# Kernel tuning notes

Hardware: AMD Instinct MI355X
Metric: run time of the kernel (lower is better)

The kernel has to match this reference:

```python
import jax, jax.numpy as jnp
import numpy as np

D_MODEL = 256
SCALE = jnp.sqrt(jnp.float32(D_MODEL))


def setup_inputs() -> dict:
    key = jax.random.key(0)
    kq, kk, kv = jax.random.split(key, 3)
    B, S, D = 4, 4096, D_MODEL
    Q = jax.random.normal(kq, (B, S, D), dtype=jnp.float32)
    K = jax.random.normal(kk, (B, S, D), dtype=jnp.float32)
    V = jax.random.normal(kv, (B, S, D), dtype=jnp.float32)
    return {"Q": Q, "K": K, "V": V}


def reference(Q, K, V):
    # scores: (B, S, S) = Q @ K^T / sqrt(d_model)
    scores = jnp.einsum('bqd,bkd->bqk', Q, K) / SCALE
    attn = jax.nn.softmax(scores, axis=-1)
    # output: (B, S, D)
    return jnp.einsum('bqk,bkd->bqd', attn, V)
```

## Files before the change

### kernel.cpp

```cpp
#include <hip/hip_runtime.h>
#include <hip/hip_bf16.h>
#include <stdint.h>

#define S_LEN 4096
#define D_DIM 256
#define NBATCH 4
#define NKT 64
#define NSUP 32

typedef unsigned short u16;
typedef float  f32x4  __attribute__((ext_vector_type(4)));
typedef __bf16 bf16x8 __attribute__((ext_vector_type(8)));
typedef __bf16 bf16x4 __attribute__((ext_vector_type(4)));
typedef short  s16x8  __attribute__((ext_vector_type(8)));
typedef short  s16x4  __attribute__((ext_vector_type(4)));

__device__ __forceinline__ f32x4 mfma16(bf16x8 a, bf16x8 b, f32x4 c) {
  return __builtin_amdgcn_mfma_f32_16x16x32_bf16(a, b, c, 0, 0, 0);
}

__device__ __forceinline__ s16x4 cvt4(float x, float y, float z, float w) {
  bf16x4 b;
  b[0] = (__bf16)x; b[1] = (__bf16)y; b[2] = (__bf16)z; b[3] = (__bf16)w;
  return __builtin_bit_cast(s16x4, b);
}

__global__ void convert_bf16_kernel(const float* __restrict__ in,
                                    u16* __restrict__ out, int n4) {
  int i = blockIdx.x * blockDim.x + threadIdx.x;
  if (i >= n4) return;
  float4 f = reinterpret_cast<const float4*>(in)[i];
  reinterpret_cast<s16x4*>(out)[i] = cvt4(f.x, f.y, f.z, f.w);
}


__device__ __forceinline__
void compute_tile(const char* KsB, const char* vpA, const char* vpB,
                  const bf16x8 (&qf)[8], f32x4 (&acc)[16],
                  float& m_run, float& l_run, int g, int h)
{
  const f32x4 fz = {0.f, 0.f, 0.f, 0.f};

  f32x4 st[4];
  __builtin_amdgcn_s_setprio(1);
  #pragma unroll
  for (int t = 0; t < 4; ++t) {
    f32x4 a = fz;
    const int row = t * 16 + h;
    const int sw  = (row & 7) << 4;
    #pragma unroll
    for (int dc = 0; dc < 8; ++dc) {
      s16x8 kfrag = *reinterpret_cast<const s16x8*>(KsB + row * 512 + ((dc * 64 + g * 16) ^ sw));
      a = mfma16(__builtin_bit_cast(bf16x8, kfrag), qf[dc], a);
    }
    st[t] = a;
  }
  __builtin_amdgcn_s_setprio(0);

  float sv[16];
  #pragma unroll
  for (int t = 0; t < 4; ++t) {
    sv[t * 4 + 0] = st[t][0]; sv[t * 4 + 1] = st[t][1];
    sv[t * 4 + 2] = st[t][2]; sv[t * 4 + 3] = st[t][3];
  }
  float tmax = sv[0];
  #pragma unroll
  for (int i = 1; i < 16; ++i) tmax = fmaxf(tmax, sv[i]);
  tmax = fmaxf(tmax, __shfl_xor(tmax, 16));
  tmax = fmaxf(tmax, __shfl_xor(tmax, 32));

  if (!__all(tmax <= m_run + 8.0f)) {
    const float mnew  = fmaxf(m_run, tmax);
    const float alpha = __expf(m_run - mnew);
    l_run *= alpha;
    const float af0 = __shfl(alpha, g * 4 + 0);
    const float af1 = __shfl(alpha, g * 4 + 1);
    const float af2 = __shfl(alpha, g * 4 + 2);
    const float af3 = __shfl(alpha, g * 4 + 3);
    #pragma unroll
    for (int dt = 0; dt < 16; ++dt) {
      acc[dt][0] *= af0; acc[dt][1] *= af1; acc[dt][2] *= af2; acc[dt][3] *= af3;
    }
    m_run = mnew;
  }

  float psum = 0.f;
  #pragma unroll
  for (int i = 0; i < 16; ++i) { sv[i] = __expf(sv[i] - m_run); psum += sv[i]; }
  psum += __shfl_xor(psum, 16);
  psum += __shfl_xor(psum, 32);
  l_run += psum;

  bf16x8 pa0, pa1;
  #pragma unroll
  for (int j = 0; j < 8; ++j) { pa0[j] = (__bf16)sv[j]; pa1[j] = (__bf16)sv[8 + j]; }

  __builtin_amdgcn_s_setprio(1);
  #pragma unroll
  for (int dt = 0; dt < 16; ++dt) {
    s16x8 v0 = *reinterpret_cast<const s16x8*>(vpA + dt * 2048);
    s16x8 v1 = *reinterpret_cast<const s16x8*>(vpB + dt * 2048);
    acc[dt] = mfma16(pa0, __builtin_bit_cast(bf16x8, v0), acc[dt]);
    acc[dt] = mfma16(pa1, __builtin_bit_cast(bf16x8, v1), acc[dt]);
  }
  __builtin_amdgcn_s_setprio(0);
}

__device__ __forceinline__
void stage_tile(int T, const u16* ksrc, char* kdst,
                const u16* vsrc, char* VtB, int Xw, int dcq)
{
  const size_t nb = (size_t)T * 64 * D_DIM;
  s16x8 kreg[8], vlo[4], vhi[4];
  #pragma unroll
  for (int i = 0; i < 8; ++i)
    kreg[i] = *reinterpret_cast<const s16x8*>(ksrc + nb + (size_t)i * 8 * D_DIM);
  #pragma unroll
  for (int r = 0; r < 4; ++r) {
    const u16* s = vsrc + nb + (size_t)r * D_DIM;
    vlo[r] = *reinterpret_cast<const s16x8*>(s);
    vhi[r] = *reinterpret_cast<const s16x8*>(s + 8);
  }
  #pragma unroll
  for (int i = 0; i < 8; ++i)
    *reinterpret_cast<s16x8*>(kdst + i * 4096) = kreg[i];
  #pragma unroll
  for (int j = 0; j < 8; ++j) {
    s16x4 c0, c1;
    c0[0] = vlo[0][j]; c0[1] = vlo[1][j]; c0[2] = vlo[2][j]; c0[3] = vlo[3][j];
    c1[0] = vhi[0][j]; c1[1] = vhi[1][j]; c1[2] = vhi[2][j]; c1[3] = vhi[3][j];
    const int d0 = dcq * 16 + j;
    const int d1 = d0 + 8;
    *reinterpret_cast<s16x4*>(VtB + d0 * 128 + (Xw ^ ((d0 & 7) << 4))) = c0;
    *reinterpret_cast<s16x4*>(VtB + d1 * 128 + (Xw ^ ((d1 & 7) << 4))) = c1;
  }
}

template<bool USE_WS>
__global__ __launch_bounds__(512, 1)
void attn_fwd_kernel(const float* __restrict__ Qg, const void* __restrict__ Kp,
                     const void* __restrict__ Vp, float* __restrict__ Og)
{
  __shared__ __align__(16) char smem[131072];

  const int wg   = blockIdx.x;
  const int swz  = (wg & 7) * 32 + (wg >> 3);
  const int b    = swz >> 6;
  const int qt   = swz & 63;
  const int tid  = threadIdx.x;
  const int wave = tid >> 6;
  const int lane = tid & 63;
  const int g    = lane >> 4;
  const int h    = lane & 15;
  const int gid  = tid >> 8;
  const int ltid = tid & 255;
  const int wq   = wave & 3;

  const int kb  = ltid & 15;
  const int dcq = ltid >> 4;
  const int Xw  = 32 * (kb & 3) + 8 * (kb >> 2);

  char* KsB = smem + gid * 65536;
  char* VtB = KsB + 32768;

  const int qbase = qt * 64 + wq * 16;

  bf16x8 qf[8];
  {
    const float* qrow = Qg + ((size_t)b * S_LEN + qbase + h) * D_DIM;
    #pragma unroll
    for (int dc = 0; dc < 8; ++dc) {
      float4 f0 = *reinterpret_cast<const float4*>(qrow + dc * 32 + g * 8);
      float4 f1 = *reinterpret_cast<const float4*>(qrow + dc * 32 + g * 8 + 4);
      bf16x8 q;
      q[0] = (__bf16)(f0.x * 0.0625f); q[1] = (__bf16)(f0.y * 0.0625f);
      q[2] = (__bf16)(f0.z * 0.0625f); q[3] = (__bf16)(f0.w * 0.0625f);
      q[4] = (__bf16)(f1.x * 0.0625f); q[5] = (__bf16)(f1.y * 0.0625f);
      q[6] = (__bf16)(f1.z * 0.0625f); q[7] = (__bf16)(f1.w * 0.0625f);
      qf[dc] = q;
    }
  }

  f32x4 acc[16];
  const f32x4 fz = {0.f, 0.f, 0.f, 0.f};
  #pragma unroll
  for (int i = 0; i < 16; ++i) acc[i] = fz;
  float m_run = -1e30f;
  float l_run = 0.f;

  const char* vpA = VtB + h * 128 + ((32 * g)      ^ ((h & 7) << 4));
  const char* vpB = VtB + h * 128 + ((32 * g + 16) ^ ((h & 7) << 4));

  if constexpr (USE_WS) {
    const u16* Kb = (const u16*)Kp + (size_t)b * S_LEN * D_DIM;
    const u16* Vb = (const u16*)Vp + (size_t)b * S_LEN * D_DIM;

    const u16* ksrc = Kb + (size_t)(ltid >> 5) * D_DIM + (ltid & 31) * 8;
    char*      kdst = KsB + (ltid >> 5) * 512 + (((ltid & 31) * 16) ^ ((ltid >> 5) << 4));
    const u16* vsrc = Vb + (size_t)(kb * 4) * D_DIM + dcq * 16;

    if (gid == 0) stage_tile(0, ksrc, kdst, vsrc, VtB, Xw, dcq);
    __syncthreads();

    for (int s = 0; s < NSUP; ++s) {
      if (gid == 0) compute_tile(KsB, vpA, vpB, qf, acc, m_run, l_run, g, h);
      else          stage_tile(2 * s + 1, ksrc, kdst, vsrc, VtB, Xw, dcq);
      __syncthreads();
      if (gid == 0) { if (s < NSUP - 1) stage_tile(2 * s + 2, ksrc, kdst, vsrc, VtB, Xw, dcq); }
      else          compute_tile(KsB, vpA, vpB, qf, acc, m_run, l_run, g, h);
      __syncthreads();
    }

  } else {
    const float* Kf = (const float*)Kp + (size_t)b * S_LEN * D_DIM;
    const float* Vf = (const float*)Vp + (size_t)b * S_LEN * D_DIM;
    for (int s = 0; s < NSUP; ++s) {
      const int kt = 2 * s + gid;
      __syncthreads();
      #pragma unroll
      for (int i = 0; i < 16; ++i) {
        int flat = i * 256 + ltid;
        int kk = flat >> 6;
        int d  = (flat & 63) * 4;
        float4 fk = *reinterpret_cast<const float4*>(Kf + (size_t)(kt * 64 + kk) * D_DIM + d);
        *reinterpret_cast<s16x4*>(KsB + kk * 512 + ((d * 2) ^ ((kk & 7) << 4))) = cvt4(fk.x, fk.y, fk.z, fk.w);
      }
      {
        s16x8 lo[4], hi[4];
        #pragma unroll
        for (int r = 0; r < 4; ++r) {
          const float* src = Vf + (size_t)(kt * 64 + kb * 4 + r) * D_DIM + dcq * 16;
          float4 f0 = *reinterpret_cast<const float4*>(src);
          float4 f1 = *reinterpret_cast<const float4*>(src + 4);
          float4 f2 = *reinterpret_cast<const float4*>(src + 8);
          float4 f3 = *reinterpret_cast<const float4*>(src + 12);
          lo[r] = __builtin_shufflevector(cvt4(f0.x, f0.y, f0.z, f0.w),
                                          cvt4(f1.x, f1.y, f1.z, f1.w), 0, 1, 2, 3, 4, 5, 6, 7);
          hi[r] = __builtin_shufflevector(cvt4(f2.x, f2.y, f2.z, f2.w),
                                          cvt4(f3.x, f3.y, f3.z, f3.w), 0, 1, 2, 3, 4, 5, 6, 7);
        }
        #pragma unroll
        for (int j = 0; j < 8; ++j) {
          s16x4 c0, c1;
          c0[0] = lo[0][j]; c0[1] = lo[1][j]; c0[2] = lo[2][j]; c0[3] = lo[3][j];
          c1[0] = hi[0][j]; c1[1] = hi[1][j]; c1[2] = hi[2][j]; c1[3] = hi[3][j];
          const int d0 = dcq * 16 + j;
          const int d1 = d0 + 8;
          *reinterpret_cast<s16x4*>(VtB + d0 * 128 + (Xw ^ ((d0 & 7) << 4))) = c0;
          *reinterpret_cast<s16x4*>(VtB + d1 * 128 + (Xw ^ ((d1 & 7) << 4))) = c1;
        }
      }
      __syncthreads();
      compute_tile(KsB, vpA, vpB, qf, acc, m_run, l_run, g, h);
    }
  }

  __syncthreads();
  float2* mlM = reinterpret_cast<float2*>(smem + 65536);
  if (gid == 1) {
    const int bw = wave - 4;
    char* base = smem + bw * 16384 + lane * 256;
    #pragma unroll
    for (int dt = 0; dt < 16; ++dt) {
      float4 v; v.x = acc[dt][0]; v.y = acc[dt][1]; v.z = acc[dt][2]; v.w = acc[dt][3];
      *reinterpret_cast<float4*>(base + (dt * 16 ^ ((lane & 7) << 4))) = v;
    }
    if (g == 0) { float2 ml; ml.x = m_run; ml.y = l_run; mlM[bw * 16 + h] = ml; }
  }
  __syncthreads();
  if (gid == 0) {
    const float2 ml = mlM[wave * 16 + h];
    const float mB = ml.x, lB = ml.y;
    const float m  = fmaxf(m_run, mB);
    const float sA = __expf(m_run - m);
    const float sB = __expf(mB - m);
    const float l  = l_run * sA + lB * sB;
    float aA[4], aB[4], inv[4];
    #pragma unroll
    for (int r = 0; r < 4; ++r) {
      aA[r]  = __shfl(sA, g * 4 + r);
      aB[r]  = __shfl(sB, g * 4 + r);
      inv[r] = 1.f / __shfl(l, g * 4 + r);
    }
    const char* base = smem + wave * 16384 + lane * 256;
    float* orow0 = Og + ((size_t)b * S_LEN + qbase) * D_DIM;
    #pragma unroll
    for (int dt = 0; dt < 16; ++dt) {
      float4 ab = *reinterpret_cast<const float4*>(base + (dt * 16 ^ ((lane & 7) << 4)));
      orow0[(size_t)(g * 4 + 0) * D_DIM + h + dt * 16] = (acc[dt][0] * aA[0] + ab.x * aB[0]) * inv[0];
      orow0[(size_t)(g * 4 + 1) * D_DIM + h + dt * 16] = (acc[dt][1] * aA[1] + ab.y * aB[1]) * inv[1];
      orow0[(size_t)(g * 4 + 2) * D_DIM + h + dt * 16] = (acc[dt][2] * aA[2] + ab.z * aB[2]) * inv[2];
      orow0[(size_t)(g * 4 + 3) * D_DIM + h + dt * 16] = (acc[dt][3] * aA[3] + ab.w * aB[3]) * inv[3];
    }
  }
}

extern "C" void kernel_launch(void* const* d_in, const int* in_sizes, int n_in,
                              void* d_out, int out_size, void* d_ws, size_t ws_size,
                              hipStream_t stream)
{
  const float* Q = (const float*)d_in[0];
  const float* K = (const float*)d_in[1];
  const float* V = (const float*)d_in[2];
  float* O = (float*)d_out;

  const size_t nelem = (size_t)NBATCH * S_LEN * D_DIM;
  const size_t need  = 2 * nelem * sizeof(u16);

  if (ws_size >= need) {
    u16* Kb = (u16*)d_ws;
    u16* Vb = Kb + nelem;
    int n4 = (int)(nelem / 4);
    convert_bf16_kernel<<<n4 / 256, 256, 0, stream>>>(K, Kb, n4);
    convert_bf16_kernel<<<n4 / 256, 256, 0, stream>>>(V, Vb, n4);
    attn_fwd_kernel<true><<<256, 512, 0, stream>>>(Q, (const void*)Kb, (const void*)Vb, O);
  } else {
    attn_fwd_kernel<false><<<256, 512, 0, stream>>>(Q, (const void*)K, (const void*)V, O);
  }
}
```

Baseline: 134.0 us.

## Pre-swizzle K/V tiles into LDS image layout and stage via global_load_lds

The bf16 conversion kernels now also write K and V as per-tile images already in the swizzled (and, for V, transposed) LDS layout. The attention kernel then copies each tile straight from global memory into LDS with global_load_lds, removing the register round trip and the per-element transpose during staging. This moves the transpose cost into the prep kernel, which uses its own LDS pass. It relies on the image layout matching exactly what compute_tile reads, and on async LDS loads being complete by the existing barriers.

Measured after the change: 126.1 us. 5.9% less time.

```diff
diff --git a/kernel.cpp b/kernel.cpp
--- a/kernel.cpp
+++ b/kernel.cpp
@@ -5,7 +5,6 @@
 #define S_LEN 4096
 #define D_DIM 256
 #define NBATCH 4
-#define NKT 64
 #define NSUP 32
 
 typedef unsigned short u16;
@@ -15,6 +14,9 @@
 typedef short  s16x8  __attribute__((ext_vector_type(8)));
 typedef short  s16x4  __attribute__((ext_vector_type(4)));
 
+#define AS1 __attribute__((address_space(1)))
+#define AS3 __attribute__((address_space(3)))
+
 __device__ __forceinline__ f32x4 mfma16(bf16x8 a, bf16x8 b, f32x4 c) {
   return __builtin_amdgcn_mfma_f32_16x16x32_bf16(a, b, c, 0, 0, 0);
 }
@@ -25,14 +27,66 @@
   return __builtin_bit_cast(s16x4, b);
 }
 
-__global__ void convert_bf16_kernel(const float* __restrict__ in,
-                                    u16* __restrict__ out, int n4) {
-  int i = blockIdx.x * blockDim.x + threadIdx.x;
-  if (i >= n4) return;
-  float4 f = reinterpret_cast<const float4*>(in)[i];
-  reinterpret_cast<s16x4*>(out)[i] = cvt4(f.x, f.y, f.z, f.w);
-}
-
+__device__ __forceinline__ void gload16(const void* g, void* l) {
+  __builtin_amdgcn_global_load_lds((const AS1 unsigned int*)g,
+                                   (AS3 unsigned int*)l, 16, 0, 0);
+}
+
+
+__global__ void build_kimg(const float* __restrict__ K, u16* __restrict__ img) {
+  const int wg  = blockIdx.x;
+  const int tid = threadIdx.x;
+  const float* src = K + (size_t)wg * 64 * D_DIM;
+  u16*         dst = img + (size_t)wg * 16384;
+  #pragma unroll
+  for (int i = 0; i < 8; ++i) {
+    const int idx = i * 256 + tid;
+    const int k = idx >> 5, p = idx & 31;
+    const int q = p ^ (k & 7);
+    const float* s = src + k * 256 + q * 8;
+    float4 f0 = *reinterpret_cast<const float4*>(s);
+    float4 f1 = *reinterpret_cast<const float4*>(s + 4);
+    s16x8 v = __builtin_shufflevector(cvt4(f0.x, f0.y, f0.z, f0.w),
+                                      cvt4(f1.x, f1.y, f1.z, f1.w),
+                                      0, 1, 2, 3, 4, 5, 6, 7);
+    *reinterpret_cast<s16x8*>(dst + k * 256 + p * 8) = v;
+  }
+}
+
+__global__ void build_vimg(const float* __restrict__ V, u16* __restrict__ img) {
+  __shared__ u16 lds[64 * 264];
+  const int wg  = blockIdx.x;
+  const int tid = threadIdx.x;
+  const float* src = V + (size_t)wg * 64 * D_DIM;
+  u16*         dst = img + (size_t)wg * 16384;
+  #pragma unroll
+  for (int i = 0; i < 8; ++i) {
+    const int idx = i * 256 + tid;
+    const int k = idx >> 5, q = idx & 31;
+    const float* s = src + k * 256 + q * 8;
+    float4 f0 = *reinterpret_cast<const float4*>(s);
+    float4 f1 = *reinterpret_cast<const float4*>(s + 4);
+    s16x8 v = __builtin_shufflevector(cvt4(f0.x, f0.y, f0.z, f0.w),
+                                      cvt4(f1.x, f1.y, f1.z, f1.w),
+                                      0, 1, 2, 3, 4, 5, 6, 7);
+    *reinterpret_cast<s16x8*>(&lds[k * 264 + q * 8]) = v;
+  }
+  __syncthreads();
+  #pragma unroll
+  for (int i = 0; i < 8; ++i) {
+    const int idx = i * 256 + tid;
+    const int d = idx >> 3, c = idx & 7;
+    const int cp = c ^ (d & 7);
+    s16x8 o;
+    #pragma unroll
+    for (int j = 0; j < 8; ++j) {
+      const int col = 8 * cp + j;
+      const int k = (col & 3) + 4 * (col >> 4) + 16 * ((col >> 2) & 3);
+      o[j] = (short)lds[k * 264 + d];
+    }
+    *reinterpret_cast<s16x8*>(dst + d * 64 + c * 8) = o;
+  }
+}
 
 __device__ __forceinline__
 void compute_tile(const char* KsB, const char* vpA, const char* vpB,
@@ -107,32 +161,16 @@
 }
 
 __device__ __forceinline__
-void stage_tile(int T, const u16* ksrc, char* kdst,
-                const u16* vsrc, char* VtB, int Xw, int dcq)
+void stage_img(const u16* KimgB, const u16* VimgB, int T,
+               char* KsB, char* VtB, int w, int lane)
 {
-  const size_t nb = (size_t)T * 64 * D_DIM;
-  s16x8 kreg[8], vlo[4], vhi[4];
-  #pragma unroll
-  for (int i = 0; i < 8; ++i)
-    kreg[i] = *reinterpret_cast<const s16x8*>(ksrc + nb + (size_t)i * 8 * D_DIM);
-  #pragma unroll
-  for (int r = 0; r < 4; ++r) {
-    const u16* s = vsrc + nb + (size_t)r * D_DIM;
-    vlo[r] = *reinterpret_cast<const s16x8*>(s);
-    vhi[r] = *reinterpret_cast<const s16x8*>(s + 8);
-  }
-  #pragma unroll
-  for (int i = 0; i < 8; ++i)
-    *reinterpret_cast<s16x8*>(kdst + i * 4096) = kreg[i];
-  #pragma unroll
-  for (int j = 0; j < 8; ++j) {
-    s16x4 c0, c1;
-    c0[0] = vlo[0][j]; c0[1] = vlo[1][j]; c0[2] = vlo[2][j]; c0[3] = vlo[3][j];
-    c1[0] = vhi[0][j]; c1[1] = vhi[1][j]; c1[2] = vhi[2][j]; c1[3] = vhi[3][j];
-    const int d0 = dcq * 16 + j;
-    const int d1 = d0 + 8;
-    *reinterpret_cast<s16x4*>(VtB + d0 * 128 + (Xw ^ ((d0 & 7) << 4))) = c0;
-    *reinterpret_cast<s16x4*>(VtB + d1 * 128 + (Xw ^ ((d1 & 7) << 4))) = c1;
+  const char* ks = (const char*)(KimgB + (size_t)T * 16384) + lane * 16;
+  const char* vs = (const char*)(VimgB + (size_t)T * 16384) + lane * 16;
+  #pragma unroll
+  for (int i = 0; i < 8; ++i) {
+    const int off = (i * 4 + w) * 1024;
+    gload16(ks + off, KsB + off);
+    gload16(vs + off, VtB + off);
   }
 }
 
@@ -155,6 +193,7 @@
   const int gid  = tid >> 8;
   const int ltid = tid & 255;
   const int wq   = wave & 3;
+  const int w    = wave & 3;
 
   const int kb  = ltid & 15;
   const int dcq = ltid >> 4;
@@ -192,21 +231,17 @@
   const char* vpB = VtB + h * 128 + ((32 * g + 16) ^ ((h & 7) << 4));
 
   if constexpr (USE_WS) {
-    const u16* Kb = (const u16*)Kp + (size_t)b * S_LEN * D_DIM;
-    const u16* Vb = (const u16*)Vp + (size_t)b * S_LEN * D_DIM;
-
-    const u16* ksrc = Kb + (size_t)(ltid >> 5) * D_DIM + (ltid & 31) * 8;
-    char*      kdst = KsB + (ltid >> 5) * 512 + (((ltid & 31) * 16) ^ ((ltid >> 5) << 4));
-    const u16* vsrc = Vb + (size_t)(kb * 4) * D_DIM + dcq * 16;
-
-    if (gid == 0) stage_tile(0, ksrc, kdst, vsrc, VtB, Xw, dcq);
+    const u16* KimgB = (const u16*)Kp + (size_t)b * 64 * 16384;
+    const u16* VimgB = (const u16*)Vp + (size_t)b * 64 * 16384;
+
+    if (gid == 0) stage_img(KimgB, VimgB, 0, KsB, VtB, w, lane);
     __syncthreads();
 
     for (int s = 0; s < NSUP; ++s) {
       if (gid == 0) compute_tile(KsB, vpA, vpB, qf, acc, m_run, l_run, g, h);
-      else          stage_tile(2 * s + 1, ksrc, kdst, vsrc, VtB, Xw, dcq);
+      else          stage_img(KimgB, VimgB, 2 * s + 1, KsB, VtB, w, lane);
       __syncthreads();
-      if (gid == 0) { if (s < NSUP - 1) stage_tile(2 * s + 2, ksrc, kdst, vsrc, VtB, Xw, dcq); }
+      if (gid == 0) { if (s < NSUP - 1) stage_img(KimgB, VimgB, 2 * s + 2, KsB, VtB, w, lane); }
       else          compute_tile(KsB, vpA, vpB, qf, acc, m_run, l_run, g, h);
       __syncthreads();
     }
@@ -308,12 +343,11 @@
   const size_t need  = 2 * nelem * sizeof(u16);
 
   if (ws_size >= need) {
-    u16* Kb = (u16*)d_ws;
-    u16* Vb = Kb + nelem;
-    int n4 = (int)(nelem / 4);
-    convert_bf16_kernel<<<n4 / 256, 256, 0, stream>>>(K, Kb, n4);
-    convert_bf16_kernel<<<n4 / 256, 256, 0, stream>>>(V, Vb, n4);
-    attn_fwd_kernel<true><<<256, 512, 0, stream>>>(Q, (const void*)Kb, (const void*)Vb, O);
+    u16* Kimg = (u16*)d_ws;
+    u16* Vimg = Kimg + nelem;
+    build_kimg<<<256, 256, 0, stream>>>(K, Kimg);
+    build_vimg<<<256, 256, 0, stream>>>(V, Vimg);
+    attn_fwd_kernel<true><<<256, 512, 0, stream>>>(Q, (const void*)Kimg, (const void*)Vimg, O);
   } else {
     attn_fwd_kernel<false><<<256, 512, 0, stream>>>(Q, (const void*)K, (const void*)V, O);
   }
```
